# Optimization experiments

Measured on AMD Instinct MI355X. Metric: run time of the kernel, lower is better.

Reference implementation:

```python
import jax, jax.numpy as jnp
import numpy as np

NUM_HEADS = 32
HEAD_DIM = 128
ROPE_THETA = 10000.0


def _rope_tables(seq_len, head_dim, dtype):
    # inv freqs: 1 / theta^(2k/d), k = 0..d/2-1
    k = jnp.arange(head_dim // 2, dtype=jnp.float32)
    inv_freq = 1.0 / (ROPE_THETA ** (2.0 * k / head_dim))
    m = jnp.arange(seq_len, dtype=jnp.float32)
    freqs = jnp.outer(m, inv_freq)  # [S, D/2]
    return jnp.cos(freqs).astype(dtype), jnp.sin(freqs).astype(dtype)


def _apply_rope(x, cos, sin):
    # x: [B, H, S, D]; pairs are (x[2k], x[2k+1]) viewed as complex
    x0 = x[..., 0::2]
    x1 = x[..., 1::2]
    # broadcast cos/sin [S, D/2] -> [1, 1, S, D/2]
    out0 = x0 * cos - x1 * sin
    out1 = x0 * sin + x1 * cos
    # re-interleave
    return jnp.stack([out0, out1], axis=-1).reshape(x.shape)


def setup_inputs() -> dict:
    key = jax.random.key(0)
    k1, k2, k3 = jax.random.split(key, 3)
    B, S, D = 2, 2048, 4096
    x = jax.random.normal(k1, (B, S, D), dtype=jnp.float32)
    w_qkv = jax.random.normal(k2, (D, 3 * D), dtype=jnp.float32) * (D ** -0.5)
    w_proj = jax.random.normal(k3, (D, D), dtype=jnp.float32) * (D ** -0.5)
    b_proj = jnp.zeros((D,), dtype=jnp.float32)
    return {"x": x, "w_qkv": w_qkv, "w_proj": w_proj, "b_proj": b_proj}


def reference(x, w_qkv, w_proj, b_proj):
    B, S, D = x.shape
    H, Hd = NUM_HEADS, HEAD_DIM

    qkv = x @ w_qkv                                   # [B, S, 3D]
    qkv = qkv.reshape(B, S, 3, H, Hd)
    qkv = jnp.transpose(qkv, (2, 0, 3, 1, 4))          # [3, B, H, S, Hd]
    q, k, v = qkv[0], qkv[1], qkv[2]

    cos, sin = _rope_tables(S, Hd, x.dtype)
    q = _apply_rope(q, cos, sin)
    k = _apply_rope(k, cos, sin)

    scale = 1.0 / np.sqrt(Hd)
    scores = jnp.einsum('bhqd,bhkd->bhqk', q, k) * scale   # [B, H, S, S]
    causal = jnp.tril(jnp.ones((S, S), dtype=bool))
    scores = jnp.where(causal, scores, jnp.finfo(scores.dtype).min)
    attn = jax.nn.softmax(scores, axis=-1)
    out = jnp.einsum('bhqk,bhkd->bhqd', attn, v)            # [B, H, S, Hd]

    ctx = jnp.transpose(out, (0, 2, 1, 3)).reshape(B, S, H * Hd)
    return ctx @ w_proj + b_proj
```

## Files before the change

kernel.cpp:

```cpp
#include <hip/hip_runtime.h>
#include <stdint.h>

typedef unsigned short ushort_t;
typedef __attribute__((ext_vector_type(8))) short s16x8;
typedef __attribute__((ext_vector_type(4))) float f32x4;
typedef __attribute__((ext_vector_type(4))) unsigned short u16x4;

#define DEV __device__ __forceinline__

DEV ushort_t f2bf(float f) {
  union { float f; uint32_t u; } v; v.f = f;
  uint32_t r = (v.u + 0x7FFFu + ((v.u >> 16) & 1u)) >> 16;
  return (ushort_t)r;
}
DEV float bf2f(ushort_t u) {
  union { uint32_t u; float f; } v; v.u = ((uint32_t)u) << 16;
  return v.f;
}

#define GLD_LDS16(g, l)                                     \
  __builtin_amdgcn_global_load_lds(                         \
      (const __attribute__((address_space(1))) void*)(g),   \
      (__attribute__((address_space(3))) void*)(l), 16, 0, 0)

#define MFMA16(a, b, c) __builtin_amdgcn_mfma_f32_16x16x32_bf16((a), (b), (c), 0, 0, 0)

__global__ __launch_bounds__(256) void k_conv(const float* __restrict__ in,
                                              ushort_t* __restrict__ out, int n4) {
  int i = blockIdx.x * 256 + threadIdx.x;
  if (i >= n4) return;
  float4 v = ((const float4*)in)[i];
  u16x4 o;
  o[0] = f2bf(v.x); o[1] = f2bf(v.y); o[2] = f2bf(v.z); o[3] = f2bf(v.w);
  *((u16x4*)out + i) = o;
}

__global__ __launch_bounds__(256) void k_transpose_conv(const float* __restrict__ in,
                                                        ushort_t* __restrict__ out,
                                                        int R, int C) {
  __shared__ float tile[64][65];
  int c0 = blockIdx.x * 64, r0 = blockIdx.y * 64;
  int t = threadIdx.x;
#pragma unroll
  for (int i = 0; i < 4; ++i) {
    int e = (i * 256 + t) * 4;
    int rr = e >> 6, cc = e & 63;
    float4 v = *(const float4*)(in + (size_t)(r0 + rr) * C + (c0 + cc));
    tile[rr][cc] = v.x; tile[rr][cc + 1] = v.y;
    tile[rr][cc + 2] = v.z; tile[rr][cc + 3] = v.w;
  }
  __syncthreads();
#pragma unroll
  for (int i = 0; i < 4; ++i) {
    int e = (i * 256 + t) * 4;
    int cc = e >> 6, rr = e & 63;
    u16x4 o;
    o[0] = f2bf(tile[rr][cc]);     o[1] = f2bf(tile[rr + 1][cc]);
    o[2] = f2bf(tile[rr + 2][cc]); o[3] = f2bf(tile[rr + 3][cc]);
    *(u16x4*)(out + (size_t)(c0 + cc) * R + (r0 + rr)) = o;
  }
}

template <bool BF16OUT, bool ROPE>
__global__ __launch_bounds__(512, 2) void k_gemm_bt(const ushort_t* __restrict__ A,
                                                    const ushort_t* __restrict__ Bt,
                                                    ushort_t* __restrict__ Cb,
                                                    float* __restrict__ Cf,
                                                    const float* __restrict__ bias,
                                                    int M, int N, int K) {
  __shared__ __align__(16) ushort_t lA[4 * 256 * 32];
  __shared__ __align__(16) ushort_t lB[4 * 256 * 32];
  int t = threadIdx.x;
  int wv = t >> 6, lane = t & 63, quad = lane >> 4, lrow = lane & 15;
  int wr = wv >> 2, wc = wv & 3;

  int nbx = gridDim.x;
  int nwg = nbx * gridDim.y;
  int id = blockIdx.y * nbx + blockIdx.x;
  int qq = nwg >> 3;
  int sw = (id & 7) * qq + (id >> 3);
  int n0 = (sw % nbx) * 256;
  int m0 = (sw / nbx) * 256;

  int srow = t >> 2;
  int gch = (t & 3) ^ ((t >> 3) & 3);
  const ushort_t* gA0 = A + (size_t)(m0 + srow) * K + gch * 8;
  const ushort_t* gA1 = gA0 + (size_t)128 * K;
  const ushort_t* gB0 = Bt + (size_t)(n0 + srow) * K + gch * 8;
  const ushort_t* gB1 = gB0 + (size_t)128 * K;
  int ldst = wv * 512;

  int xorv = (lrow >> 1) & 3;
  int aoff = (wr * 128 + lrow) * 32 + ((quad ^ xorv) * 8);
  int boff = (wc * 64 + lrow) * 32 + ((quad ^ xorv) * 8);

  f32x4 acc[8][4];
#pragma unroll
  for (int i = 0; i < 8; ++i)
#pragma unroll
    for (int j = 0; j < 4; ++j) acc[i][j] = (f32x4){0.f, 0.f, 0.f, 0.f};

  int nt = K >> 5;

  auto stageA = [&](int tt) {
    int buf = tt & 3;
    size_t ko = (size_t)tt * 32;
    ushort_t* la = lA + buf * 8192 + ldst;
    GLD_LDS16(gA0 + ko, la);
    GLD_LDS16(gA1 + ko, la + 4096);
  };
  auto stageB = [&](int tt) {
    int buf = tt & 3;
    size_t ko = (size_t)tt * 32;
    ushort_t* lb = lB + buf * 8192 + ldst;
    GLD_LDS16(gB0 + ko, lb);
    GLD_LDS16(gB1 + ko, lb + 4096);
  };

  stageA(0); stageB(0);
  stageA(1); stageB(1);
  stageA(2); stageB(2);

#define TILE_BODY(BUFV, DOSTAGE, TT)                                     \
  {                                                                      \
    const ushort_t* ba = lA + (BUFV) * 8192;                             \
    const ushort_t* bb = lB + (BUFV) * 8192;                             \
    s16x8 af[4], bfr[4];                                                 \
    _Pragma("unroll") for (int j = 0; j < 4; ++j)                        \
        bfr[j] = *(const s16x8*)(bb + boff + j * 512);                   \
    _Pragma("unroll") for (int i = 0; i < 4; ++i)                        \
        af[i] = *(const s16x8*)(ba + aoff + i * 512);                    \
    if (DOSTAGE) stageA((TT) + 3);                                       \
    __builtin_amdgcn_s_setprio(1);                                       \
    _Pragma("unroll") for (int i = 0; i < 4; ++i)                        \
      _Pragma("unroll") for (int j = 0; j < 4; ++j)                      \
          acc[i][j] = MFMA16(af[i], bfr[j], acc[i][j]);                  \
    __builtin_amdgcn_s_setprio(0);                                       \
    _Pragma("unroll") for (int i = 0; i < 4; ++i)                        \
        af[i] = *(const s16x8*)(ba + aoff + (i + 4) * 512);              \
    if (DOSTAGE) stageB((TT) + 3);                                       \
    __builtin_amdgcn_s_setprio(1);                                       \
    _Pragma("unroll") for (int i = 0; i < 4; ++i)                        \
      _Pragma("unroll") for (int j = 0; j < 4; ++j)                      \
          acc[i + 4][j] = MFMA16(af[i], bfr[j], acc[i + 4][j]);          \
    __builtin_amdgcn_s_setprio(0);                                       \
  }

  for (int tt = 0; tt < nt - 2; ++tt) {
    asm volatile("s_waitcnt vmcnt(8)" ::: "memory");
    __builtin_amdgcn_s_barrier();
    TILE_BODY(tt & 3, (tt < nt - 3), tt);
  }
  asm volatile("s_waitcnt vmcnt(4)" ::: "memory");
  __builtin_amdgcn_s_barrier();
  TILE_BODY((nt - 2) & 3, false, nt - 2);
  asm volatile("s_waitcnt vmcnt(0)" ::: "memory");
  __builtin_amdgcn_s_barrier();
  TILE_BODY((nt - 1) & 3, false, nt - 1);
#undef TILE_BODY

  bool do_rope = ROPE && (n0 < 8192);
  float sgn_sel = (lrow & 1) ? 1.f : -1.f;
#pragma unroll
  for (int j = 0; j < 4; ++j) {
    int gc = n0 + wc * 64 + j * 16 + lrow;
    float freq = 0.f;
    if (do_rope) {
      int p = (gc & 127) >> 1;
      freq = __expf(-(float)p * 0.14391156509165667f);
    }
#pragma unroll
    for (int i = 0; i < 8; ++i)
#pragma unroll
      for (int r = 0; r < 4; ++r) {
        int gr = m0 + wr * 128 + i * 16 + quad * 4 + r;
        float val = acc[i][j][r];
        if (do_rope) {
          float other = __shfl_xor(val, 1);
          float sv, cv;
          sincosf((float)(gr & 2047) * freq, &sv, &cv);
          val = fmaf(other, sgn_sel * sv, val * cv);
        }
        if (BF16OUT)
          Cb[(size_t)gr * N + gc] = f2bf(val);
        else
          Cf[(size_t)gr * N + gc] = val + bias[gc];
      }
  }
}

__global__ __launch_bounds__(256) void k_build_vt(const ushort_t* __restrict__ qkv,
                                                  ushort_t* __restrict__ vt) {
  const int S = 2048;
  int s0 = blockIdx.x * 64;
  int bh = blockIdx.y;
  int b = bh >> 5, h = bh & 31;
  __shared__ ushort_t tl[64][136];
  int t = threadIdx.x;
  const ushort_t* src = qkv + (size_t)(b * S + s0) * 12288 + 8192 + h * 128;
#pragma unroll
  for (int i = 0; i < 4; ++i) {
    int e = (i * 256 + t) * 8;
    int row = e >> 7, col = e & 127;
    *(s16x8*)&tl[row][col] = *(const s16x8*)(src + (size_t)row * 12288 + col);
  }
  __syncthreads();
  ushort_t* dst = vt + (size_t)bh * 128 * S;
#pragma unroll
  for (int i = 0; i < 4; ++i) {
    int e = (i * 256 + t) * 8;
    int d = e >> 6, ss = e & 63;
    s16x8 o;
#pragma unroll
    for (int j = 0; j < 8; ++j) o[j] = (short)tl[ss + j][d];
    *(s16x8*)(dst + (size_t)d * S + s0 + ss) = o;
  }
}

__global__ __launch_bounds__(256, 2) void k_attn(const ushort_t* __restrict__ qkv,
                                                 const ushort_t* __restrict__ vt,
                                                 ushort_t* __restrict__ ctx) {
  const int S = 2048;
  int qt = blockIdx.x, bh = blockIdx.y;
  int b = bh >> 5, h = bh & 31;
  int q0 = qt * 128;
  int t = threadIdx.x;
  int wv = t >> 6, lane = t & 63, quad = lane >> 4, lrow = lane & 15;

  __shared__ ushort_t lK[64 * 128];
  __shared__ ushort_t lV[128 * 64];
  __shared__ ushort_t lP[4][32][72];

  const ushort_t* qp = qkv + (size_t)(b * S) * 12288 + h * 128;
  const ushort_t* kp = qp + 4096;
  const ushort_t* vp = vt + (size_t)bh * 128 * S;

  s16x8 qf[2][4];
  int qrb = q0 + wv * 32;
#pragma unroll
  for (int ti = 0; ti < 2; ++ti)
#pragma unroll
    for (int ks = 0; ks < 4; ++ks)
      qf[ti][ks] = *(const s16x8*)(qp + (size_t)(qrb + ti * 16 + lrow) * 12288 +
                                   ks * 32 + quad * 8);

  f32x4 O[2][8];
#pragma unroll
  for (int ti = 0; ti < 2; ++ti)
#pragma unroll
    for (int f = 0; f < 8; ++f) O[ti][f] = (f32x4){0.f, 0.f, 0.f, 0.f};
  float m_i[2][4], l_i[2][4];
#pragma unroll
  for (int ti = 0; ti < 2; ++ti)
#pragma unroll
    for (int r = 0; r < 4; ++r) { m_i[ti][r] = -__builtin_inff(); l_i[ti][r] = 0.f; }

  const float scale = 0.08838834764831845f;
  int qhi = q0 + 127;

  for (int kv0 = 0; kv0 <= qhi; kv0 += 64) {
    __syncthreads();
    {
      int ck = lane & 15;
      int cv = lane & 7;
#pragma unroll
      for (int it = 0; it < 4; ++it) {
        int slot = wv * 4 + it;
        int rowk = slot * 4 + (lane >> 4);
        int cpk = (ck & 8) | ((ck & 7) ^ (rowk & 7));
        GLD_LDS16(kp + (size_t)(kv0 + rowk) * 12288 + cpk * 8, lK + slot * 512);
        int rowv = slot * 8 + (lane >> 3);
        int cpv = cv ^ (rowv & 7);
        GLD_LDS16(vp + (size_t)rowv * S + kv0 + cpv * 8, lV + slot * 512);
      }
    }
    __syncthreads();

    f32x4 sc[2][4];
#pragma unroll
    for (int ti = 0; ti < 2; ++ti)
#pragma unroll
      for (int nt = 0; nt < 4; ++nt) sc[ti][nt] = (f32x4){0.f, 0.f, 0.f, 0.f};
#pragma unroll
    for (int ks = 0; ks < 4; ++ks) {
      s16x8 bk[4];
#pragma unroll
      for (int nt = 0; nt < 4; ++nt) {
        int row = nt * 16 + lrow;
        int cc = ks * 4 + quad;
        int cp = (cc & 8) | ((cc & 7) ^ (row & 7));
        bk[nt] = *(const s16x8*)(lK + row * 128 + cp * 8);
      }
#pragma unroll
      for (int ti = 0; ti < 2; ++ti)
#pragma unroll
        for (int nt = 0; nt < 4; ++nt) sc[ti][nt] = MFMA16(qf[ti][ks], bk[nt], sc[ti][nt]);
    }

#pragma unroll
    for (int ti = 0; ti < 2; ++ti) {
      int qr = qrb + ti * 16 + quad * 4;
      float mt[4];
#pragma unroll
      for (int r = 0; r < 4; ++r) mt[r] = -__builtin_inff();
      float pvl[4][4];
#pragma unroll
      for (int nt = 0; nt < 4; ++nt) {
        int kc = kv0 + nt * 16 + lrow;
#pragma unroll
        for (int r = 0; r < 4; ++r) {
          float sv = sc[ti][nt][r] * scale;
          if (kc > qr + r) sv = -__builtin_inff();
          pvl[nt][r] = sv;
          mt[r] = fmaxf(mt[r], sv);
        }
      }
#pragma unroll
      for (int r = 0; r < 4; ++r)
#pragma unroll
        for (int off = 1; off < 16; off <<= 1)
          mt[r] = fmaxf(mt[r], __shfl_xor(mt[r], off, 16));

      float al[4], ls[4];
#pragma unroll
      for (int r = 0; r < 4; ++r) {
        float mn = fmaxf(m_i[ti][r], mt[r]);
        al[r] = __expf(m_i[ti][r] - mn);
        m_i[ti][r] = mn;
        ls[r] = 0.f;
      }
#pragma unroll
      for (int nt = 0; nt < 4; ++nt)
#pragma unroll
        for (int r = 0; r < 4; ++r) {
          float p = __expf(pvl[nt][r] - m_i[ti][r]);
          ushort_t pu = f2bf(p);
          lP[wv][ti * 16 + quad * 4 + r][nt * 16 + lrow] = pu;
          ls[r] += bf2f(pu);
        }
#pragma unroll
      for (int r = 0; r < 4; ++r) {
#pragma unroll
        for (int off = 1; off < 16; off <<= 1) ls[r] += __shfl_xor(ls[r], off, 16);
        l_i[ti][r] = al[r] * l_i[ti][r] + ls[r];
      }
#pragma unroll
      for (int f = 0; f < 8; ++f)
#pragma unroll
        for (int r = 0; r < 4; ++r) O[ti][f][r] *= al[r];
    }

#pragma unroll
    for (int ks = 0; ks < 2; ++ks) {
      s16x8 pa[2];
#pragma unroll
      for (int ti = 0; ti < 2; ++ti)
        pa[ti] = *(const s16x8*)&lP[wv][ti * 16 + lrow][ks * 32 + quad * 8];
#pragma unroll
      for (int f = 0; f < 8; ++f) {
        int row = f * 16 + lrow;
        int cc = ks * 4 + quad;
        int cp = cc ^ (row & 7);
        s16x8 bv = *(const s16x8*)(lV + row * 64 + cp * 8);
#pragma unroll
        for (int ti = 0; ti < 2; ++ti) O[ti][f] = MFMA16(pa[ti], bv, O[ti][f]);
      }
    }
  }

#pragma unroll
  for (int ti = 0; ti < 2; ++ti) {
    float inv[4];
#pragma unroll
    for (int r = 0; r < 4; ++r) inv[r] = 1.f / l_i[ti][r];
#pragma unroll
    for (int f = 0; f < 8; ++f)
#pragma unroll
      for (int r = 0; r < 4; ++r) {
        size_t idx = (size_t)(b * S + qrb + ti * 16 + quad * 4 + r) * 4096 +
                     h * 128 + f * 16 + lrow;
        ctx[idx] = f2bf(O[ti][f][r] * inv[r]);
      }
  }
}

extern "C" void kernel_launch(void* const* d_in, const int* in_sizes, int n_in,
                              void* d_out, int out_size, void* d_ws, size_t ws_size,
                              hipStream_t stream) {
  const float* x      = (const float*)d_in[0];
  const float* w_qkv  = (const float*)d_in[1];
  const float* w_proj = (const float*)d_in[2];
  const float* b_proj = (const float*)d_in[3];
  float* out = (float*)d_out;

  char* ws = (char*)d_ws;
  ushort_t* xb     = (ushort_t*)(ws);
  ushort_t* wqkvt  = (ushort_t*)(ws + 33554432ULL);
  ushort_t* wprojt = (ushort_t*)(ws + 134217728ULL);
  ushort_t* qkvb   = (ushort_t*)(ws + 167772160ULL);
  ushort_t* vt     = (ushort_t*)(ws + 268435456ULL);
  ushort_t* ctx    = (ushort_t*)(ws + 301989888ULL);

  k_conv<<<16384, 256, 0, stream>>>(x, xb, 16777216 / 4);
  k_transpose_conv<<<dim3(192, 64), 256, 0, stream>>>(w_qkv, wqkvt, 4096, 12288);
  k_transpose_conv<<<dim3(64, 64), 256, 0, stream>>>(w_proj, wprojt, 4096, 4096);
  k_gemm_bt<true, true><<<dim3(48, 16), 512, 0, stream>>>(xb, wqkvt, qkvb, nullptr,
                                                          nullptr, 4096, 12288, 4096);
  k_build_vt<<<dim3(32, 64), 256, 0, stream>>>(qkvb, vt);
  k_attn<<<dim3(16, 64), 256, 0, stream>>>(qkvb, vt, ctx);
  k_gemm_bt<false, false><<<dim3(16, 16), 512, 0, stream>>>(ctx, wprojt, nullptr, out,
                                                            b_proj, 4096, 4096, 4096);
}
```

Baseline: 1.356 ms.

## Split GEMM tile body into two barrier-synchronized phases ping-pong style

```diff
diff --git a/kernel.cpp b/kernel.cpp
--- a/kernel.cpp
+++ b/kernel.cpp
@@ -117,47 +117,64 @@
     GLD_LDS16(gB1 + ko, lb + 4096);
   };
 
-  stageA(0); stageB(0);
-  stageA(1); stageB(1);
-  stageA(2); stageB(2);
-
-#define TILE_BODY(BUFV, DOSTAGE, TT)                                     \
+  s16x8 af[4], bfr[4];
+
+#define PHASE_A(BUFV, DOSTAGE, TT)                                       \
   {                                                                      \
     const ushort_t* ba = lA + (BUFV) * 8192;                             \
     const ushort_t* bb = lB + (BUFV) * 8192;                             \
-    s16x8 af[4], bfr[4];                                                 \
     _Pragma("unroll") for (int j = 0; j < 4; ++j)                        \
         bfr[j] = *(const s16x8*)(bb + boff + j * 512);                   \
     _Pragma("unroll") for (int i = 0; i < 4; ++i)                        \
         af[i] = *(const s16x8*)(ba + aoff + i * 512);                    \
     if (DOSTAGE) stageA((TT) + 3);                                       \
+    __builtin_amdgcn_s_barrier();                                        \
+    asm volatile("s_waitcnt lgkmcnt(0)" ::: "memory");                   \
+    __builtin_amdgcn_sched_barrier(0);                                   \
     __builtin_amdgcn_s_setprio(1);                                       \
     _Pragma("unroll") for (int i = 0; i < 4; ++i)                        \
       _Pragma("unroll") for (int j = 0; j < 4; ++j)                      \
           acc[i][j] = MFMA16(af[i], bfr[j], acc[i][j]);                  \
     __builtin_amdgcn_s_setprio(0);                                       \
+    __builtin_amdgcn_s_barrier();                                        \
+  }
+
+#define PHASE_B(BUFV, DOSTAGE, TT, VMWAIT)                               \
+  {                                                                      \
+    const ushort_t* ba = lA + (BUFV) * 8192;                             \
     _Pragma("unroll") for (int i = 0; i < 4; ++i)                        \
         af[i] = *(const s16x8*)(ba + aoff + (i + 4) * 512);              \
     if (DOSTAGE) stageB((TT) + 3);                                       \
+    VMWAIT;                                                              \
+    __builtin_amdgcn_s_barrier();                                        \
+    asm volatile("s_waitcnt lgkmcnt(0)" ::: "memory");                   \
+    __builtin_amdgcn_sched_barrier(0);                                   \
     __builtin_amdgcn_s_setprio(1);                                       \
     _Pragma("unroll") for (int i = 0; i < 4; ++i)                        \
       _Pragma("unroll") for (int j = 0; j < 4; ++j)                      \
           acc[i + 4][j] = MFMA16(af[i], bfr[j], acc[i + 4][j]);          \
     __builtin_amdgcn_s_setprio(0);                                       \
-  }
-
-  for (int tt = 0; tt < nt - 2; ++tt) {
-    asm volatile("s_waitcnt vmcnt(8)" ::: "memory");
-    __builtin_amdgcn_s_barrier();
-    TILE_BODY(tt & 3, (tt < nt - 3), tt);
-  }
-  asm volatile("s_waitcnt vmcnt(4)" ::: "memory");
+    __builtin_amdgcn_s_barrier();                                        \
+  }
+
+  stageA(0); stageB(0);
+  stageA(1); stageB(1);
+  stageA(2); stageB(2);
+  asm volatile("s_waitcnt vmcnt(8)" ::: "memory");
   __builtin_amdgcn_s_barrier();
-  TILE_BODY((nt - 2) & 3, false, nt - 2);
-  asm volatile("s_waitcnt vmcnt(0)" ::: "memory");
-  __builtin_amdgcn_s_barrier();
-  TILE_BODY((nt - 1) & 3, false, nt - 1);
-#undef TILE_BODY
+
+  for (int tt = 0; tt < nt - 3; ++tt) {
+    PHASE_A(tt & 3, true, tt);
+    PHASE_B(tt & 3, true, tt, asm volatile("s_waitcnt vmcnt(8)" ::: "memory"));
+  }
+  PHASE_A((nt - 3) & 3, false, 0);
+  PHASE_B((nt - 3) & 3, false, 0, asm volatile("s_waitcnt vmcnt(4)" ::: "memory"));
+  PHASE_A((nt - 2) & 3, false, 0);
+  PHASE_B((nt - 2) & 3, false, 0, asm volatile("s_waitcnt vmcnt(0)" ::: "memory"));
+  PHASE_A((nt - 1) & 3, false, 0);
+  PHASE_B((nt - 1) & 3, false, 0, (void)0);
+#undef PHASE_A
+#undef PHASE_B
 
   bool do_rope = ROPE && (n0 < 8192);
   float sgn_sel = (lrow & 1) ? 1.f : -1.f;
```

Result: slower. 1.570 ms (+15.8%).

## Double-buffer K/V tiles in attention, remap block order, swizzle P buffer

Applied to the files above, without the earlier changes.

```diff
diff --git a/kernel.cpp b/kernel.cpp
--- a/kernel.cpp
+++ b/kernel.cpp
@@ -221,15 +221,17 @@
                                                  const ushort_t* __restrict__ vt,
                                                  ushort_t* __restrict__ ctx) {
   const int S = 2048;
-  int qt = blockIdx.x, bh = blockIdx.y;
+  int p = blockIdx.y * 16 + blockIdx.x;
+  int w = (p & 7) * 128 + (p >> 3);
+  int qt = w & 15, bh = w >> 4;
   int b = bh >> 5, h = bh & 31;
   int q0 = qt * 128;
   int t = threadIdx.x;
   int wv = t >> 6, lane = t & 63, quad = lane >> 4, lrow = lane & 15;
 
-  __shared__ ushort_t lK[64 * 128];
-  __shared__ ushort_t lV[128 * 64];
-  __shared__ ushort_t lP[4][32][72];
+  __shared__ __align__(16) ushort_t lK[2][64 * 128];
+  __shared__ __align__(16) ushort_t lV[2][128 * 64];
+  __shared__ __align__(16) ushort_t lP[4][32][64];
 
   const ushort_t* qp = qkv + (size_t)(b * S) * 12288 + h * 128;
   const ushort_t* kp = qp + 4096;
@@ -256,25 +258,41 @@
     for (int r = 0; r < 4; ++r) { m_i[ti][r] = -__builtin_inff(); l_i[ti][r] = 0.f; }
 
   const float scale = 0.08838834764831845f;
-  int qhi = q0 + 127;
-
-  for (int kv0 = 0; kv0 <= qhi; kv0 += 64) {
-    __syncthreads();
-    {
-      int ck = lane & 15;
-      int cv = lane & 7;
-#pragma unroll
-      for (int it = 0; it < 4; ++it) {
-        int slot = wv * 4 + it;
-        int rowk = slot * 4 + (lane >> 4);
-        int cpk = (ck & 8) | ((ck & 7) ^ (rowk & 7));
-        GLD_LDS16(kp + (size_t)(kv0 + rowk) * 12288 + cpk * 8, lK + slot * 512);
-        int rowv = slot * 8 + (lane >> 3);
-        int cpv = cv ^ (rowv & 7);
-        GLD_LDS16(vp + (size_t)rowv * S + kv0 + cpv * 8, lV + slot * 512);
-      }
-    }
-    __syncthreads();
+  int NT = qt * 2 + 2;
+
+  auto stage = [&](int tt) {
+    int kv0 = tt * 64;
+    int bo = (tt & 1) * 8192;
+    int ck = lane & 15;
+    int cv = lane & 7;
+#pragma unroll
+    for (int it = 0; it < 4; ++it) {
+      int slot = wv * 4 + it;
+      int rowk = slot * 4 + (lane >> 4);
+      int cpk = (ck & 8) | ((ck & 7) ^ (rowk & 7));
+      GLD_LDS16(kp + (size_t)(kv0 + rowk) * 12288 + cpk * 8, &lK[0][0] + bo + slot * 512);
+      int rowv = slot * 8 + (lane >> 3);
+      int cpv = cv ^ (rowv & 7);
+      GLD_LDS16(vp + (size_t)rowv * S + kv0 + cpv * 8, &lV[0][0] + bo + slot * 512);
+    }
+  };
+
+  stage(0);
+
+  for (int tt = 0; tt < NT; ++tt) {
+    int kv0 = tt * 64;
+    const ushort_t* Kb = &lK[tt & 1][0];
+    const ushort_t* Vb = &lV[tt & 1][0];
+
+    asm volatile("s_waitcnt lgkmcnt(0)" ::: "memory");
+    __builtin_amdgcn_s_barrier();
+    if (tt + 1 < NT) {
+      stage(tt + 1);
+      asm volatile("s_waitcnt vmcnt(8)" ::: "memory");
+    } else {
+      asm volatile("s_waitcnt vmcnt(0)" ::: "memory");
+    }
+    __builtin_amdgcn_s_barrier();
 
     f32x4 sc[2][4];
 #pragma unroll
@@ -289,12 +307,14 @@
         int row = nt * 16 + lrow;
         int cc = ks * 4 + quad;
         int cp = (cc & 8) | ((cc & 7) ^ (row & 7));
-        bk[nt] = *(const s16x8*)(lK + row * 128 + cp * 8);
-      }
+        bk[nt] = *(const s16x8*)(Kb + row * 128 + cp * 8);
+      }
+      __builtin_amdgcn_s_setprio(1);
 #pragma unroll
       for (int ti = 0; ti < 2; ++ti)
 #pragma unroll
         for (int nt = 0; nt < 4; ++nt) sc[ti][nt] = MFMA16(qf[ti][ks], bk[nt], sc[ti][nt]);
+      __builtin_amdgcn_s_setprio(0);
     }
 
 #pragma unroll
@@ -333,9 +353,11 @@
       for (int nt = 0; nt < 4; ++nt)
 #pragma unroll
         for (int r = 0; r < 4; ++r) {
-          float p = __expf(pvl[nt][r] - m_i[ti][r]);
-          ushort_t pu = f2bf(p);
-          lP[wv][ti * 16 + quad * 4 + r][nt * 16 + lrow] = pu;
+          float pexp = __expf(pvl[nt][r] - m_i[ti][r]);
+          ushort_t pu = f2bf(pexp);
+          int prow = quad * 4 + r;
+          lP[wv][ti * 16 + prow]
+            [(((nt * 2 + (lrow >> 3)) ^ (prow & 7)) << 3) | (lrow & 7)] = pu;
           ls[r] += bf2f(pu);
         }
 #pragma unroll
@@ -355,15 +377,18 @@
       s16x8 pa[2];
 #pragma unroll
       for (int ti = 0; ti < 2; ++ti)
-        pa[ti] = *(const s16x8*)&lP[wv][ti * 16 + lrow][ks * 32 + quad * 8];
+        pa[ti] = *(const s16x8*)&lP[wv][ti * 16 + lrow]
+                     [(((ks * 4 + quad) ^ (lrow & 7)) << 3)];
 #pragma unroll
       for (int f = 0; f < 8; ++f) {
         int row = f * 16 + lrow;
         int cc = ks * 4 + quad;
         int cp = cc ^ (row & 7);
-        s16x8 bv = *(const s16x8*)(lV + row * 64 + cp * 8);
+        s16x8 bv = *(const s16x8*)(Vb + row * 64 + cp * 8);
+        __builtin_amdgcn_s_setprio(1);
 #pragma unroll
         for (int ti = 0; ti < 2; ++ti) O[ti][f] = MFMA16(pa[ti], bv, O[ti][f]);
+        __builtin_amdgcn_s_setprio(0);
       }
     }
   }
```

New measurement: 1.271 ms. 6.2% less time.
